# Performance work log

Hardware: AMD Instinct MI355X
Metric: run time of the kernel (lower is better)

Reference implementation:

```python
import jax, jax.numpy as jnp
import numpy as np

B, S, D = 4, 2048, 1024
H = 16
HD = D // H  # 64


def setup_inputs() -> dict:
    key = jax.random.key(0)
    kx, kq, kp = jax.random.split(key, 3)
    x = jax.random.normal(kx, (B, S, D), dtype=jnp.float32)
    # torch Linear weights are [out, in]; match init scale ~ U(-1/sqrt(in), 1/sqrt(in))
    lim = 1.0 / np.sqrt(D)
    w_qkv = jax.random.uniform(kq, (3 * D, D), dtype=jnp.float32, minval=-lim, maxval=lim)
    w_proj = jax.random.uniform(kp, (D, D), dtype=jnp.float32, minval=-lim, maxval=lim)
    return {"x": x, "w_qkv": w_qkv, "w_proj": w_proj}


def reference(x, w_qkv, w_proj):
    b, s, d = x.shape
    qkv = jnp.einsum('bsd,ed->bse', x, w_qkv)  # [B,S,3D]
    q, k, v = jnp.split(qkv, 3, axis=-1)
    # [B,H,S,HD]
    q = q.reshape(b, s, H, HD).transpose(0, 2, 1, 3)
    k = k.reshape(b, s, H, HD).transpose(0, 2, 1, 3)
    v = v.reshape(b, s, H, HD).transpose(0, 2, 1, 3)
    scale = 1.0 / np.sqrt(HD)
    attn = jnp.einsum('bhqd,bhkd->bhqk', q, k) * scale  # [B,H,S,S]
    causal = jnp.tril(jnp.ones((s, s), dtype=bool))
    attn = jnp.where(causal[None, None], attn, -jnp.inf)
    attn = jax.nn.softmax(attn, axis=-1)
    out = jnp.einsum('bhqk,bhkd->bhqd', attn, v)
    out = out.transpose(0, 2, 1, 3).reshape(b, s, d)
    return jnp.einsum('bsd,ed->bse', out, w_proj)
```

## Files before the change

### kernel.cpp

```cpp
#include <hip/hip_runtime.h>

typedef unsigned short u16;
typedef unsigned int u32;

#define B_ 4
#define S_ 2048
#define D_ 1024
#define H_ 16
#define HD_ 64
#define M_ (B_ * S_)
#define QK_ (2 * D_)

typedef __bf16 bf16x8 __attribute__((ext_vector_type(8)));
typedef float f32x4 __attribute__((ext_vector_type(4)));

#define MASKVAL (-1.0e30f)
#define RESCALE_THR 8.0f

static __device__ __forceinline__ u16 f2bf_hw(float f) {
    union { __bf16 b; u16 u; } v;
    v.b = (__bf16)f;
    return v.u;
}

static __device__ __forceinline__ void gload16(const u16* g, u16* l) {
    __builtin_amdgcn_global_load_lds(
        (const __attribute__((address_space(1))) void*)g,
        (__attribute__((address_space(3))) void*)l, 16, 0, 0);
}

__global__ __launch_bounds__(256) void cvt_bf16(const float* __restrict__ src,
                                                u16* __restrict__ dst) {
    size_t i = ((size_t)blockIdx.x * 256 + threadIdx.x) * 8;
    float4 a = *(const float4*)(src + i);
    float4 b = *(const float4*)(src + i + 4);
    union { u16 h[8]; int4 v; } pk;
    pk.h[0] = f2bf_hw(a.x); pk.h[1] = f2bf_hw(a.y);
    pk.h[2] = f2bf_hw(a.z); pk.h[3] = f2bf_hw(a.w);
    pk.h[4] = f2bf_hw(b.x); pk.h[5] = f2bf_hw(b.y);
    pk.h[6] = f2bf_hw(b.z); pk.h[7] = f2bf_hw(b.w);
    *(int4*)(dst + i) = pk.v;
}

template <int EPI>
__global__ __launch_bounds__(256) void gemm_bb(const u16* __restrict__ A,
                                               const u16* __restrict__ Bw,
                                               void* __restrict__ Cout,
                                               void* __restrict__ C2,
                                               int Ndim, int Kdim) {
    __shared__ u16 Alds[128 * 64];
    __shared__ u16 Blds[128 * 64];
    const int t = threadIdx.x;
    const int bx = blockIdx.x, by = blockIdx.y;
    const int wave = t >> 6, lane = t & 63;
    const int ml = lane & 15, quad = lane >> 4;
    const int wm = (wave >> 1) * 64, wn = (wave & 1) * 64;
    const int rowA0 = by * 128, rowB0 = bx * 128;
    const int sr8 = lane >> 3;
    const int sc8 = (lane & 7) * 8;

    f32x4 acc[4][4];
    const f32x4 zero = {0.f, 0.f, 0.f, 0.f};
#pragma unroll
    for (int i = 0; i < 4; ++i)
#pragma unroll
        for (int j = 0; j < 4; ++j) acc[i][j] = zero;

    for (int k0 = 0; k0 < Kdim; k0 += 64) {
        __syncthreads();
#pragma unroll
        for (int p = 0; p < 4; ++p) {
            const int rbase = wave * 32 + p * 8;
            gload16(&A[(size_t)(rowA0 + rbase + sr8) * Kdim + k0 + sc8],
                    &Alds[rbase * 64]);
            gload16(&Bw[(size_t)(rowB0 + rbase + sr8) * Kdim + k0 + sc8],
                    &Blds[rbase * 64]);
        }
        __syncthreads();
#pragma unroll
        for (int kc = 0; kc < 2; ++kc) {
            bf16x8 a[4], b[4];
#pragma unroll
            for (int i = 0; i < 4; ++i)
                a[i] = *(const bf16x8*)(&Alds[(wm + i * 16 + ml) * 64 + kc * 32 + quad * 8]);
#pragma unroll
            for (int j = 0; j < 4; ++j)
                b[j] = *(const bf16x8*)(&Blds[(wn + j * 16 + ml) * 64 + kc * 32 + quad * 8]);
#pragma unroll
            for (int i = 0; i < 4; ++i)
#pragma unroll
                for (int j = 0; j < 4; ++j)
                    acc[i][j] = __builtin_amdgcn_mfma_f32_16x16x32_bf16(a[i], b[j], acc[i][j], 0, 0, 0);
        }
    }

    const bool doVt = (EPI == 1) || (EPI == 3 && bx >= 16);
    if ((EPI == 0) || (EPI == 3 && !doVt)) {
        u16* C = (u16*)Cout;
#pragma unroll
        for (int i = 0; i < 4; ++i)
#pragma unroll
            for (int j = 0; j < 4; ++j)
#pragma unroll
                for (int r = 0; r < 4; ++r) {
                    int row = rowA0 + wm + i * 16 + quad * 4 + r;
                    int col = rowB0 + wn + j * 16 + ml;
                    C[(size_t)row * Ndim + col] = f2bf_hw(acc[i][j][r]);
                }
    } else if (doVt) {
        u16* Vt = (EPI == 3) ? (u16*)C2 : (u16*)Cout;
        const int voff = (EPI == 3) ? 2048 : 0;
#pragma unroll
        for (int i = 0; i < 4; ++i)
#pragma unroll
            for (int j = 0; j < 4; ++j) {
                int row0 = rowA0 + wm + i * 16 + quad * 4;
                int col = rowB0 + wn + j * 16 + ml - voff;
                int b = row0 >> 11;
                int s0 = row0 & (S_ - 1);
                union { u16 h[4]; ushort4 v; } pk;
#pragma unroll
                for (int r = 0; r < 4; ++r) pk.h[r] = f2bf_hw(acc[i][j][r]);
                *(ushort4*)(&Vt[((size_t)(b * D_ + col)) * S_ + s0]) = pk.v;
            }
    } else {
        float* C = (float*)Cout;
#pragma unroll
        for (int i = 0; i < 4; ++i)
#pragma unroll
            for (int j = 0; j < 4; ++j)
#pragma unroll
                for (int r = 0; r < 4; ++r) {
                    int row = rowA0 + wm + i * 16 + quad * 4 + r;
                    int col = rowB0 + wn + j * 16 + ml;
                    C[(size_t)row * Ndim + col] = acc[i][j][r];
                }
    }
}

__global__ __launch_bounds__(256, 3) void attn3(const u16* __restrict__ qk,
                                                const u16* __restrict__ Vt,
                                                u16* __restrict__ AO) {
    __shared__ u16 Klds[2][64 * 64];
    __shared__ u16 Vlds[2][64 * 64];
    __shared__ u16 Pw[4][32 * 72];
    const int t = threadIdx.x;
    const int wave = t >> 6, lane = t & 63;
    const int ml = lane & 15, quad = lane >> 4;
    const int mhx = (ml & 8) >> 1;

    const int jj = blockIdx.x >> 6;
    const int bh = blockIdx.x & 63;
    const int t4 = jj >> 2, r4 = jj & 3;
    const int j = (t4 < 2) ? (15 - 4 * t4 - r4) : (12 - 4 * t4 + r4);
    const int b = bh >> 4, h = bh & 15;
    const size_t rowbase = (size_t)b * S_;

    const int srow8 = lane >> 3;
    const int schunk = ((lane & 7) ^ srow8) * 8;

    const int qj0 = j * 128 + wave * 32;
    const int ktw = 2 * j + (wave >> 1);
    const int ktmax = 2 * j + 1;

    u16* pwb = &Pw[wave][0];

    bf16x8 qf[2][2];
#pragma unroll
    for (int mi = 0; mi < 2; ++mi)
#pragma unroll
        for (int kc = 0; kc < 2; ++kc) {
            bf16x8 q = *(const bf16x8*)(&qk[(rowbase + qj0 + mi * 16 + ml) * QK_ +
                                            h * HD_ + kc * 32 + quad * 8]);
#pragma unroll
            for (int e = 0; e < 8; ++e) {
                float f = (float)q[e] * 0.125f;
                q[e] = (__bf16)f;
            }
            qf[mi][kc] = q;
        }

    f32x4 o[2][4];
    float m[2], ls[2];
    const f32x4 zero = {0.f, 0.f, 0.f, 0.f};
#pragma unroll
    for (int mi = 0; mi < 2; ++mi) {
#pragma unroll
        for (int nd = 0; nd < 4; ++nd) o[mi][nd] = zero;
        m[mi] = MASKVAL; ls[mi] = 0.f;
    }

    bf16x8 vf[4][2];

    auto STAGE = [&](int buf, int kt) {
        const int kb = kt * 64;
#pragma unroll
        for (int p = 0; p < 2; ++p) {
            const int rbase = wave * 16 + p * 8;
            gload16(&qk[(rowbase + kb + rbase + srow8) * QK_ + D_ + h * HD_ + schunk],
                    &Klds[buf][rbase * 64]);
            gload16(&Vt[(size_t)(bh * HD_ + rbase + srow8) * S_ + kb + schunk],
                    &Vlds[buf][rbase * 64]);
        }
    };

    auto PV = [&]() {
        bf16x8 pf[2][2];
#pragma unroll
        for (int mi = 0; mi < 2; ++mi)
#pragma unroll
            for (int kc = 0; kc < 2; ++kc)
                pf[mi][kc] = *(const bf16x8*)(&pwb[(mi * 16 + ml) * 72 +
                                                   (((kc * 4 + quad) ^ mhx) << 3)]);
        __builtin_amdgcn_s_setprio(1);
#pragma unroll
        for (int mi = 0; mi < 2; ++mi)
#pragma unroll
            for (int nd = 0; nd < 4; ++nd)
#pragma unroll
                for (int kc = 0; kc < 2; ++kc)
                    o[mi][nd] = __builtin_amdgcn_mfma_f32_16x16x32_bf16(pf[mi][kc], vf[nd][kc],
                                                                        o[mi][nd], 0, 0, 0);
        __builtin_amdgcn_s_setprio(0);
    };

    STAGE(0, 0);

    for (int kt = 0; kt <= ktmax; ++kt) {
        const int cur = kt & 1;
        if (kt < ktmax) STAGE(cur ^ 1, kt + 1);

        if (kt >= 1 && kt - 1 <= ktw) PV();

        if (kt < ktmax) {
            asm volatile("s_waitcnt vmcnt(4)" ::: "memory");
        } else {
            asm volatile("s_waitcnt vmcnt(0)" ::: "memory");
        }
        __builtin_amdgcn_s_barrier();

        if (kt <= ktw) {
            const int kb = kt * 64;
            f32x4 sc[2][4];
            __builtin_amdgcn_s_setprio(1);
#pragma unroll
            for (int ni = 0; ni < 4; ++ni) {
                const int row = ni * 16 + ml;
                bf16x8 kfa = *(const bf16x8*)(&Klds[cur][row * 64 + ((quad ^ (ml & 7)) << 3)]);
                bf16x8 kfb = *(const bf16x8*)(&Klds[cur][row * 64 + (((4 + quad) ^ (ml & 7)) << 3)]);
#pragma unroll
                for (int mi = 0; mi < 2; ++mi) {
                    f32x4 s = __builtin_amdgcn_mfma_f32_16x16x32_bf16(kfa, qf[mi][0], zero, 0, 0, 0);
                    sc[mi][ni] = __builtin_amdgcn_mfma_f32_16x16x32_bf16(kfb, qf[mi][1], s, 0, 0, 0);
                }
            }
            __builtin_amdgcn_s_setprio(0);

            if (kb + 63 > qj0) {
#pragma unroll
                for (int mi = 0; mi < 2; ++mi) {
                    const int q = qj0 + mi * 16 + ml;
#pragma unroll
                    for (int ni = 0; ni < 4; ++ni)
#pragma unroll
                        for (int r = 0; r < 4; ++r) {
                            int k = kb + ni * 16 + quad * 4 + r;
                            if (k > q) sc[mi][ni][r] = MASKVAL;
                        }
                }
            }

#pragma unroll
            for (int mi = 0; mi < 2; ++mi) {
                float tm = sc[mi][0][0];
#pragma unroll
                for (int ni = 0; ni < 4; ++ni)
#pragma unroll
                    for (int r = 0; r < 4; ++r) tm = fmaxf(tm, sc[mi][ni][r]);
                tm = fmaxf(tm, __shfl_xor(tm, 16, 64));
                tm = fmaxf(tm, __shfl_xor(tm, 32, 64));
                if (__any(tm > m[mi] + RESCALE_THR)) {
                    float mn = fmaxf(m[mi], tm);
                    float al = __expf(m[mi] - mn);
                    m[mi] = mn;
                    ls[mi] *= al;
                    float alr[4];
#pragma unroll
                    for (int r = 0; r < 4; ++r)
                        alr[r] = __shfl(al, (lane & 48) + ((lane & 48) >> 2) + r, 64);
#pragma unroll
                    for (int nd = 0; nd < 4; ++nd)
#pragma unroll
                        for (int r = 0; r < 4; ++r) o[mi][nd][r] *= alr[r];
                }
                float sum = 0.f;
#pragma unroll
                for (int ni = 0; ni < 4; ++ni)
#pragma unroll
                    for (int r = 0; r < 4; ++r) {
                        float e = __expf(sc[mi][ni][r] - m[mi]);
                        sc[mi][ni][r] = e;
                        sum += e;
                    }
                ls[mi] += sum;
#pragma unroll
                for (int ni = 0; ni < 4; ++ni) {
                    union { u16 h[4]; ushort4 v; } pk;
#pragma unroll
                    for (int r = 0; r < 4; ++r) pk.h[r] = f2bf_hw(sc[mi][ni][r]);
                    const int off = (mi * 16 + ml) * 72 +
                                    ((((2 * ni + (quad >> 1)) ^ mhx)) << 3) + ((quad & 1) << 2);
                    *(ushort4*)(&pwb[off]) = pk.v;
                }
            }
#pragma unroll
            for (int ni = 0; ni < 4; ++ni) {
                const int row = ni * 16 + ml;
#pragma unroll
                for (int kc = 0; kc < 2; ++kc)
                    vf[ni][kc] = *(const bf16x8*)(&Vlds[cur][row * 64 +
                                                            (((kc * 4 + quad) ^ (ml & 7)) << 3)]);
            }
        }
        asm volatile("s_waitcnt lgkmcnt(0)" ::: "memory");
        __builtin_amdgcn_s_barrier();
    }

    if (ktw == ktmax) PV();

#pragma unroll
    for (int mi = 0; mi < 2; ++mi) {
        float s = ls[mi];
        s += __shfl_xor(s, 16, 64);
        s += __shfl_xor(s, 32, 64);
        float rl = 1.0f / s;
        float rlr[4];
#pragma unroll
        for (int r = 0; r < 4; ++r)
            rlr[r] = __shfl(rl, (lane & 48) + ((lane & 48) >> 2) + r, 64);
#pragma unroll
        for (int nd = 0; nd < 4; ++nd)
#pragma unroll
            for (int r = 0; r < 4; ++r) {
                int srow = qj0 + mi * 16 + quad * 4 + r;
                AO[(rowbase + srow) * D_ + h * HD_ + nd * 16 + ml] =
                    f2bf_hw(o[mi][nd][r] * rlr[r]);
            }
    }
}

__global__ __launch_bounds__(256) void copy16(const int4* __restrict__ src,
                                              int4* __restrict__ dst) {
    size_t i = (size_t)blockIdx.x * 256 + threadIdx.x;
    dst[i] = src[i];
}

extern "C" void kernel_launch(void* const* d_in, const int* in_sizes, int n_in,
                              void* d_out, int out_size, void* d_ws, size_t ws_size,
                              hipStream_t stream) {
    const float* x = (const float*)d_in[0];
    const float* wqkv = (const float*)d_in[1];
    const float* wproj = (const float*)d_in[2];
    float* out = (float*)d_out;

    u16* qkw = (u16*)d_ws;
    u16* Vtw = qkw + (size_t)M_ * QK_;

    u16* xb = (u16*)d_out;
    u16* wprojb = xb + (size_t)M_ * D_;
    u16* wqkvb = wprojb + (size_t)D_ * D_;

    const size_t need = ((size_t)M_ * QK_ + 8388608  + (size_t)M_ * D_  +
                         (size_t)D_ * D_ ) * sizeof(u16);
    const bool bigws = ws_size >= need;
    u16* AOb    = bigws ? (Vtw + (size_t)8388608) : xb;
    u16* wprojd = bigws ? (AOb + (size_t)M_ * D_) : wprojb;
    u16* AOp    = bigws ? AOb : qkw;
    u16* wprojp = bigws ? wprojd : qkw + (size_t)M_ * D_;

    cvt_bf16<<<dim3(M_ * D_ / 2048), 256, 0, stream>>>(x, xb);
    cvt_bf16<<<dim3(D_ * D_ / 2048), 256, 0, stream>>>(wproj, wprojd);
    cvt_bf16<<<dim3(3 * D_ * D_ / 2048), 256, 0, stream>>>(wqkv, wqkvb);

    gemm_bb<3><<<dim3(3 * D_ / 128, M_ / 128), 256, 0, stream>>>(
        xb, wqkvb, qkw, Vtw, QK_, D_);
    attn3<<<dim3(1024), 256, 0, stream>>>(qkw, Vtw, AOb);
    if (!bigws) {
        copy16<<<dim3((unsigned)(((size_t)M_ * D_ + (size_t)D_ * D_) * 2 / (256 * 16))),
                 256, 0, stream>>>((const int4*)AOb, (int4*)qkw);
    }
    gemm_bb<2><<<dim3(D_ / 128, M_ / 128), 256, 0, stream>>>(
        AOp, wprojp, out, nullptr, D_, D_);
}
```

Before: 266.7 us.

## Rewrite GEMMs as 8-wave 256x128 tiles with double-buffered swizzled LDS pipeline

Replaces the single-buffered 128x128 GEMM with a 512-thread kernel that computes a 256x128 tile per block. LDS is split into double-buffered half-K slices with an XOR swizzle. Async global-to-LDS loads for the next slice are issued while MFMAs run on the current one, using explicit vmcnt waits, barriers and setprio. The aim is to hide global load latency and cut LDS bank conflicts. In exchange, K is hardcoded to 1024, LDS use per block is larger, and the smaller grid may reduce occupancy or tail balance.

```diff
diff --git a/kernel.cpp b/kernel.cpp
--- a/kernel.cpp
+++ b/kernel.cpp
@@ -10,6 +10,7 @@
 #define HD_ 64
 #define M_ (B_ * S_)
 #define QK_ (2 * D_)
+#define NT_ 16
 
 typedef __bf16 bf16x8 __attribute__((ext_vector_type(8)));
 typedef float f32x4 __attribute__((ext_vector_type(4)));
@@ -43,21 +44,21 @@
 }
 
 template <int EPI>
-__global__ __launch_bounds__(256) void gemm_bb(const u16* __restrict__ A,
-                                               const u16* __restrict__ Bw,
-                                               void* __restrict__ Cout,
-                                               void* __restrict__ C2,
-                                               int Ndim, int Kdim) {
-    __shared__ u16 Alds[128 * 64];
-    __shared__ u16 Blds[128 * 64];
+__global__ __launch_bounds__(512, 2) void gemm8p(const u16* __restrict__ A,
+                                                 const u16* __restrict__ Bw,
+                                                 void* __restrict__ Cout,
+                                                 void* __restrict__ C2,
+                                                 int Ndim) {
+    __shared__ u16 As[2][2][256 * 32];
+    __shared__ u16 Bs[2][2][128 * 32];
     const int t = threadIdx.x;
-    const int bx = blockIdx.x, by = blockIdx.y;
     const int wave = t >> 6, lane = t & 63;
     const int ml = lane & 15, quad = lane >> 4;
-    const int wm = (wave >> 1) * 64, wn = (wave & 1) * 64;
-    const int rowA0 = by * 128, rowB0 = bx * 128;
-    const int sr8 = lane >> 3;
-    const int sc8 = (lane & 7) * 8;
+    const int wr = wave >> 1, wc = wave & 1;
+    const int bx = blockIdx.x, by = blockIdx.y;
+    const int rowA0 = by * 256, rowB0 = bx * 128;
+    const int sr = lane >> 2;
+    const int sch = ((lane & 3) ^ ((lane >> 3) & 3)) * 8;
 
     f32x4 acc[4][4];
     const f32x4 zero = {0.f, 0.f, 0.f, 0.f};
@@ -66,75 +67,119 @@
 #pragma unroll
         for (int j = 0; j < 4; ++j) acc[i][j] = zero;
 
-    for (int k0 = 0; k0 < Kdim; k0 += 64) {
-        __syncthreads();
-#pragma unroll
-        for (int p = 0; p < 4; ++p) {
-            const int rbase = wave * 32 + p * 8;
-            gload16(&A[(size_t)(rowA0 + rbase + sr8) * Kdim + k0 + sc8],
-                    &Alds[rbase * 64]);
-            gload16(&Bw[(size_t)(rowB0 + rbase + sr8) * Kdim + k0 + sc8],
-                    &Blds[rbase * 64]);
-        }
-        __syncthreads();
-#pragma unroll
-        for (int kc = 0; kc < 2; ++kc) {
+    auto STAGE_A = [&](int buf, int kt, int kc) {
+#pragma unroll
+        for (int p = 0; p < 2; ++p) {
+            const int rb = wave * 32 + p * 16;
+            gload16(&A[(size_t)(rowA0 + rb + sr) * 1024 + kt * 64 + kc * 32 + sch],
+                    &As[buf][kc][rb * 32]);
+        }
+    };
+    auto STAGE_B = [&](int buf, int kt, int kc) {
+        const int rb = wave * 16;
+        gload16(&Bw[(size_t)(rowB0 + rb + sr) * 1024 + kt * 64 + kc * 32 + sch],
+                &Bs[buf][kc][rb * 32]);
+    };
+    auto LDA = [&](int buf, int kc, int i) -> bf16x8 {
+        const int row = wr * 64 + i * 16 + ml;
+        return *(const bf16x8*)(&As[buf][kc][row * 32 + ((quad ^ ((row >> 1) & 3)) << 3)]);
+    };
+    auto LDB = [&](int buf, int kc, int j) -> bf16x8 {
+        const int row = wc * 64 + j * 16 + ml;
+        return *(const bf16x8*)(&Bs[buf][kc][row * 32 + ((quad ^ ((row >> 1) & 3)) << 3)]);
+    };
+
+    STAGE_A(0, 0, 0); STAGE_B(0, 0, 0);
+    STAGE_A(0, 0, 1); STAGE_B(0, 0, 1);
+    STAGE_A(1, 1, 0); STAGE_B(1, 1, 0);
+    asm volatile("s_waitcnt vmcnt(3)" ::: "memory");
+    __builtin_amdgcn_s_barrier();
+
+    for (int kt = 0; kt < NT_; ++kt) {
+        const int cur = kt & 1;
+        {
             bf16x8 a[4], b[4];
 #pragma unroll
-            for (int i = 0; i < 4; ++i)
-                a[i] = *(const bf16x8*)(&Alds[(wm + i * 16 + ml) * 64 + kc * 32 + quad * 8]);
-#pragma unroll
-            for (int j = 0; j < 4; ++j)
-                b[j] = *(const bf16x8*)(&Blds[(wn + j * 16 + ml) * 64 + kc * 32 + quad * 8]);
+            for (int i = 0; i < 4; ++i) a[i] = LDA(cur, 0, i);
+#pragma unroll
+            for (int j = 0; j < 4; ++j) b[j] = LDB(cur, 0, j);
+            if (kt + 1 < NT_) { STAGE_A(cur ^ 1, kt + 1, 1); STAGE_B(cur ^ 1, kt + 1, 1); }
+            __builtin_amdgcn_s_barrier();
+            asm volatile("s_waitcnt lgkmcnt(0)" ::: "memory");
+            __builtin_amdgcn_sched_barrier(0);
+            __builtin_amdgcn_s_setprio(1);
 #pragma unroll
             for (int i = 0; i < 4; ++i)
 #pragma unroll
                 for (int j = 0; j < 4; ++j)
                     acc[i][j] = __builtin_amdgcn_mfma_f32_16x16x32_bf16(a[i], b[j], acc[i][j], 0, 0, 0);
-        }
-    }
-
-    const bool doVt = (EPI == 1) || (EPI == 3 && bx >= 16);
-    if ((EPI == 0) || (EPI == 3 && !doVt)) {
-        u16* C = (u16*)Cout;
+            __builtin_amdgcn_s_setprio(0);
+            __builtin_amdgcn_s_barrier();
+        }
+        {
+            bf16x8 a[4], b[4];
+#pragma unroll
+            for (int i = 0; i < 4; ++i) a[i] = LDA(cur, 1, i);
+#pragma unroll
+            for (int j = 0; j < 4; ++j) b[j] = LDB(cur, 1, j);
+            if (kt + 2 < NT_) { STAGE_A(cur, kt + 2, 0); STAGE_B(cur, kt + 2, 0); }
+            __builtin_amdgcn_s_barrier();
+            asm volatile("s_waitcnt lgkmcnt(0)" ::: "memory");
+            __builtin_amdgcn_sched_barrier(0);
+            __builtin_amdgcn_s_setprio(1);
+#pragma unroll
+            for (int i = 0; i < 4; ++i)
+#pragma unroll
+                for (int j = 0; j < 4; ++j)
+                    acc[i][j] = __builtin_amdgcn_mfma_f32_16x16x32_bf16(a[i], b[j], acc[i][j], 0, 0, 0);
+            __builtin_amdgcn_s_setprio(0);
+            if (kt + 2 < NT_) { asm volatile("s_waitcnt vmcnt(3)" ::: "memory"); }
+            else              { asm volatile("s_waitcnt vmcnt(0)" ::: "memory"); }
+            __builtin_amdgcn_s_barrier();
+        }
+    }
+
+    if constexpr (EPI == 2) {
+        float* C = (float*)Cout;
 #pragma unroll
         for (int i = 0; i < 4; ++i)
 #pragma unroll
             for (int j = 0; j < 4; ++j)
 #pragma unroll
                 for (int r = 0; r < 4; ++r) {
-                    int row = rowA0 + wm + i * 16 + quad * 4 + r;
-                    int col = rowB0 + wn + j * 16 + ml;
-                    C[(size_t)row * Ndim + col] = f2bf_hw(acc[i][j][r]);
-                }
-    } else if (doVt) {
-        u16* Vt = (EPI == 3) ? (u16*)C2 : (u16*)Cout;
-        const int voff = (EPI == 3) ? 2048 : 0;
-#pragma unroll
-        for (int i = 0; i < 4; ++i)
-#pragma unroll
-            for (int j = 0; j < 4; ++j) {
-                int row0 = rowA0 + wm + i * 16 + quad * 4;
-                int col = rowB0 + wn + j * 16 + ml - voff;
-                int b = row0 >> 11;
-                int s0 = row0 & (S_ - 1);
-                union { u16 h[4]; ushort4 v; } pk;
-#pragma unroll
-                for (int r = 0; r < 4; ++r) pk.h[r] = f2bf_hw(acc[i][j][r]);
-                *(ushort4*)(&Vt[((size_t)(b * D_ + col)) * S_ + s0]) = pk.v;
-            }
+                    int row = rowA0 + wr * 64 + i * 16 + quad * 4 + r;
+                    int col = rowB0 + wc * 64 + j * 16 + ml;
+                    C[(size_t)row * Ndim + col] = acc[i][j][r];
+                }
     } else {
-        float* C = (float*)Cout;
-#pragma unroll
-        for (int i = 0; i < 4; ++i)
-#pragma unroll
-            for (int j = 0; j < 4; ++j)
-#pragma unroll
-                for (int r = 0; r < 4; ++r) {
-                    int row = rowA0 + wm + i * 16 + quad * 4 + r;
-                    int col = rowB0 + wn + j * 16 + ml;
-                    C[(size_t)row * Ndim + col] = acc[i][j][r];
-                }
+        if (bx < 16) {
+            u16* C = (u16*)Cout;
+#pragma unroll
+            for (int i = 0; i < 4; ++i)
+#pragma unroll
+                for (int j = 0; j < 4; ++j)
+#pragma unroll
+                    for (int r = 0; r < 4; ++r) {
+                        int row = rowA0 + wr * 64 + i * 16 + quad * 4 + r;
+                        int col = rowB0 + wc * 64 + j * 16 + ml;
+                        C[(size_t)row * Ndim + col] = f2bf_hw(acc[i][j][r]);
+                    }
+        } else {
+            u16* Vt = (u16*)C2;
+#pragma unroll
+            for (int i = 0; i < 4; ++i)
+#pragma unroll
+                for (int j = 0; j < 4; ++j) {
+                    int row0 = rowA0 + wr * 64 + i * 16 + quad * 4;
+                    int col = rowB0 + wc * 64 + j * 16 + ml - 2048;
+                    int b = row0 >> 11;
+                    int s0 = row0 & (S_ - 1);
+                    union { u16 h[4]; ushort4 v; } pk;
+#pragma unroll
+                    for (int r = 0; r < 4; ++r) pk.h[r] = f2bf_hw(acc[i][j][r]);
+                    *(ushort4*)(&Vt[((size_t)(b * D_ + col)) * S_ + s0]) = pk.v;
+                }
+        }
     }
 }
 
@@ -382,13 +427,13 @@
     cvt_bf16<<<dim3(D_ * D_ / 2048), 256, 0, stream>>>(wproj, wprojd);
     cvt_bf16<<<dim3(3 * D_ * D_ / 2048), 256, 0, stream>>>(wqkv, wqkvb);
 
-    gemm_bb<3><<<dim3(3 * D_ / 128, M_ / 128), 256, 0, stream>>>(
-        xb, wqkvb, qkw, Vtw, QK_, D_);
+    gemm8p<3><<<dim3(3 * D_ / 128, M_ / 256), 512, 0, stream>>>(
+        xb, wqkvb, qkw, Vtw, QK_);
     attn3<<<dim3(1024), 256, 0, stream>>>(qkw, Vtw, AOb);
     if (!bigws) {
         copy16<<<dim3((unsigned)(((size_t)M_ * D_ + (size_t)D_ * D_) * 2 / (256 * 16))),
                  256, 0, stream>>>((const int4*)AOb, (int4*)qkw);
     }
-    gemm_bb<2><<<dim3(D_ / 128, M_ / 128), 256, 0, stream>>>(
-        AOp, wprojp, out, nullptr, D_, D_);
-}
+    gemm8p<2><<<dim3(D_ / 128, M_ / 256), 512, 0, stream>>>(
+        AOp, wprojp, out, nullptr, D_);
+}
```

New measurement: 257.1 us. 1.04x faster.
